# Kernel optimization log

Measured on AMD Instinct MI355X. Metric: run time of the kernel, lower is better.

The kernel has to match this reference:

```python
import jax, jax.numpy as jnp
import numpy as np

N_NODES = 50000
N_EDGES = 800000
DIM = 128


def setup_inputs() -> dict:
    key = jax.random.key(0)
    k_x, k_e, k_w1, k_w2 = jax.random.split(key, 4)
    x = jax.random.normal(k_x, (N_NODES, DIM), dtype=jnp.float32)
    edge_index = jax.random.randint(k_e, (2, N_EDGES), 0, N_NODES, dtype=jnp.int64)
    scale = 1.0 / np.sqrt(DIM)
    W1 = jax.random.normal(k_w1, (DIM, DIM), dtype=jnp.float32) * scale
    b1 = jnp.zeros((DIM,), dtype=jnp.float32)
    W2 = jax.random.normal(k_w2, (DIM, DIM), dtype=jnp.float32) * scale
    b2 = jnp.zeros((DIM,), dtype=jnp.float32)
    return {"x": x, "edge_index": edge_index, "W1": W1, "b1": b1, "W2": W2, "b2": b2}


def _gcn_conv(x, W, b, src, dst, n_nodes):
    """PyG GCNConv: D^{-1/2}(A+I)D^{-1/2} (x @ W) + b, self-loops added."""
    h = x @ W  # [N, D]
    ones = jnp.ones(src.shape[0], dtype=h.dtype)
    # degree of A+I, counting incoming edges at target nodes plus self-loop
    deg = jax.ops.segment_sum(ones, dst, num_segments=n_nodes) + 1.0
    dinv = jax.lax.rsqrt(deg)  # [N]
    norm = dinv[src] * dinv[dst]  # [E]
    msgs = h[src] * norm[:, None]  # [E, D] gather (memory-bound)
    agg = jax.ops.segment_sum(msgs, dst, num_segments=n_nodes)  # scatter-add
    agg = agg + h * (dinv * dinv)[:, None]  # self-loop contribution
    return agg + b


def reference(x, edge_index, W1, b1, W2, b2):
    src, dst = edge_index[0], edge_index[1]
    n = x.shape[0]
    identity = x
    out = jax.nn.relu(_gcn_conv(x, W1, b1, src, dst, n))
    out = _gcn_conv(out, W2, b2, src, dst, n)
    return jax.nn.relu(out + identity)
```

## Files before the change

kernel.cpp:

```cpp
#include <hip/hip_runtime.h>

#define N_NODES 50000
#define N_EDGES 800000
#define DIM 128
#define NB 391
#define CAP 2560
#define NCH 7
#define BIN_CHUNK 4096
#define BIN_BLOCKS 196
#define GEMM_TILES 782
#define AGG_TILES 1563

typedef unsigned int uint;
typedef unsigned short ushort;
typedef __attribute__((ext_vector_type(8))) __bf16 bf16x8;
typedef __attribute__((ext_vector_type(4))) float f32x4;

__device__ __forceinline__ uint f2bf(float f) {
    uint u = __float_as_uint(f);
    return (u + 0x7FFFu + ((u >> 16) & 1u)) >> 16;
}
__device__ __forceinline__ float2 bf2f2(uint u) {
    return make_float2(__uint_as_float(u << 16), __uint_as_float(u & 0xFFFF0000u));
}


__global__ __launch_bounds__(256) void prep_kernel(const float* __restrict__ W1,
                                                   const float* __restrict__ W2,
                                                   uint* __restrict__ Wt1,
                                                   uint* __restrict__ Wt2,
                                                   int* __restrict__ bincursor) {
    int idx = blockIdx.x * 256 + threadIdx.x;
    if (idx < 16384) {
        const float* W = (idx < 8192) ? W1 : W2;
        uint* Wt = (idx < 8192) ? Wt1 : Wt2;
        int i = idx & 8191;
        int n = i >> 6, k2 = i & 63;
        Wt[i] = f2bf(W[(2 * k2) * DIM + n]) | (f2bf(W[(2 * k2 + 1) * DIM + n]) << 16);
    } else {
        int b = idx - 16384;
        if (b < NB) bincursor[b] = b * CAP;
    }
}


__device__ __forceinline__ void gemm_tile64(const float* __restrict__ X,
                                            const uint* __restrict__ Wt, int base,
                                            uint* __restrict__ Hout) {
    int t = threadIdx.x;
    int wv = t >> 6;
    int l = t & 63;
    int col = l & 15;
    int g = l >> 4;
    int grow = base + wv * 16 + col;
    int ar = grow > N_NODES - 1 ? N_NODES - 1 : grow;

    bf16x8 af[4];
    const float4* Xr = (const float4*)(X + (size_t)ar * DIM);
#pragma unroll
    for (int kk = 0; kk < 4; ++kk) {
        float4 x0 = Xr[kk * 8 + g * 2];
        float4 x1 = Xr[kk * 8 + g * 2 + 1];
        uint4 p;
        p.x = f2bf(x0.x) | (f2bf(x0.y) << 16);
        p.y = f2bf(x0.z) | (f2bf(x0.w) << 16);
        p.z = f2bf(x1.x) | (f2bf(x1.y) << 16);
        p.w = f2bf(x1.z) | (f2bf(x1.w) << 16);
        af[kk] = __builtin_bit_cast(bf16x8, p);
    }

    const uint4* Wr = (const uint4*)Wt;
    f32x4 acc[8];
#pragma unroll
    for (int n = 0; n < 8; ++n) acc[n] = (f32x4){0.f, 0.f, 0.f, 0.f};

#pragma unroll
    for (int n = 0; n < 8; ++n) {
        const uint4* wrow = Wr + (size_t)(n * 16 + col) * 16;
#pragma unroll
        for (int kk = 0; kk < 4; ++kk) {
            bf16x8 bf = __builtin_bit_cast(bf16x8, wrow[kk * 4 + g]);
            acc[n] = __builtin_amdgcn_mfma_f32_16x16x32_bf16(af[kk], bf, acc[n], 0, 0, 0);
        }
    }

#pragma unroll
    for (int j = 0; j < 4; ++j) {
        int row = base + wv * 16 + g * 4 + j;
        if (row < N_NODES) {
            ushort* hrow = (ushort*)(Hout + (size_t)row * 64);
#pragma unroll
            for (int n = 0; n < 8; ++n) hrow[n * 16 + col] = (ushort)f2bf(acc[n][j]);
        }
    }
}


__device__ __forceinline__ void gemm_tile32_lds(const uint* __restrict__ sB,
                                                const uint* __restrict__ Wt,
                                                const float* __restrict__ dinv, int base,
                                                uint* __restrict__ Hout) {
    int t = threadIdx.x;
    int wv = t >> 6;
    int l = t & 63;
    int col = l & 15;
    int g = l >> 4;
    int rh = wv & 1;
    int ch = wv >> 1;
    int lr = rh * 16 + col;

    bf16x8 af[4];
#pragma unroll
    for (int kk = 0; kk < 4; ++kk) {
        int ui = lr * 64 + ((kk * 16 + g * 4) ^ ((lr & 7) << 2));
        af[kk] = __builtin_bit_cast(bf16x8, *(const uint4*)&sB[ui]);
    }

    const uint4* Wr = (const uint4*)Wt;
    f32x4 acc[4];
#pragma unroll
    for (int nn = 0; nn < 4; ++nn) acc[nn] = (f32x4){0.f, 0.f, 0.f, 0.f};

#pragma unroll
    for (int nn = 0; nn < 4; ++nn) {
        int n = ch * 4 + nn;
        const uint4* wrow = Wr + (size_t)(n * 16 + col) * 16;
#pragma unroll
        for (int kk = 0; kk < 4; ++kk) {
            bf16x8 bf = __builtin_bit_cast(bf16x8, wrow[kk * 4 + g]);
            acc[nn] = __builtin_amdgcn_mfma_f32_16x16x32_bf16(af[kk], bf, acc[nn], 0, 0, 0);
        }
    }

#pragma unroll
    for (int j = 0; j < 4; ++j) {
        int row = base + rh * 16 + g * 4 + j;
        if (row < N_NODES) {
            float di = dinv[row];
            ushort* hrow = (ushort*)(Hout + (size_t)row * 64);
#pragma unroll
            for (int nn = 0; nn < 4; ++nn) {
                int n = ch * 4 + nn;
                hrow[n * 16 + col] = (ushort)f2bf(acc[nn][j] * di);
            }
        }
    }
}


__global__ __launch_bounds__(256) void bin_gemm1_kernel(const int* __restrict__ ei,
                                                        int* __restrict__ bincursor,
                                                        uint* __restrict__ pairs,
                                                        const float* __restrict__ x,
                                                        const uint* __restrict__ Wt1,
                                                        uint* __restrict__ Hs) {
    if (blockIdx.x >= BIN_BLOCKS) {
        gemm_tile64(x, Wt1, (blockIdx.x - BIN_BLOCKS) * 64, Hs);
        return;
    }
    __shared__ int lh[NB];
    __shared__ int lbase[NB];
    int t = threadIdx.x;
    int eb = blockIdx.x * BIN_CHUNK;

    for (int b = t; b < NB; b += 256) lh[b] = 0;
    __syncthreads();

    int s_reg[16], d_reg[16];
#pragma unroll
    for (int i = 0; i < 16; ++i) {
        int e = eb + i * 256 + t;
        if (e < N_EDGES) {
            s_reg[i] = ei[e];
            d_reg[i] = ei[N_EDGES + e];
            atomicAdd(&lh[d_reg[i] >> 7], 1);
        } else {
            d_reg[i] = -1;
        }
    }
    __syncthreads();

    for (int b = t; b < NB; b += 256) {
        int c = lh[b];
        lbase[b] = c ? atomicAdd(&bincursor[b], c) : 0;
    }
    __syncthreads();
    for (int b = t; b < NB; b += 256) lh[b] = 0;
    __syncthreads();

#pragma unroll
    for (int i = 0; i < 16; ++i) {
        int d = d_reg[i];
        if (d >= 0) {
            int bin = d >> 7;
            int r = atomicAdd(&lh[bin], 1);
            pairs[lbase[bin] + r] = ((uint)s_reg[i] << 7) | (uint)(d & 127);
        }
    }
}


__global__ __launch_bounds__(256) void fill2_kernel(const uint* __restrict__ pairs,
                                                    const int* __restrict__ bincursor,
                                                    int* __restrict__ rowbeg,
                                                    int* __restrict__ rowend,
                                                    float* __restrict__ dinv,
                                                    int* __restrict__ csr_src) {
    __shared__ int cnt[128 * 8];
    __shared__ int nsum[128];
    __shared__ int nbase[128];
    int t = threadIdx.x;
    int blk = blockIdx.x;
    int bs = blk * CAP;
    int be = bincursor[blk];

    for (int i = t; i < 128 * 8; i += 256) cnt[i] = 0;
    __syncthreads();

    for (int p = bs + t; p < be; p += 256) {
        uint pr = pairs[p];
        atomicAdd(&cnt[(pr & 127u) * 8 + (pr >> 20)], 1);
    }
    __syncthreads();

    if (t < 128) {
        int s = 0;
#pragma unroll
        for (int c = 0; c < NCH; ++c) s += cnt[t * 8 + c];
        nsum[t] = s;
        nbase[t] = s;
    }
    __syncthreads();
#pragma unroll
    for (int off = 1; off < 128; off <<= 1) {
        int v = (t < 128 && t >= off) ? nbase[t - off] : 0;
        __syncthreads();
        if (t < 128) nbase[t] += v;
        __syncthreads();
    }

    if (t < 128) {
        int ex = nbase[t] - nsum[t];
        int node = blk * 128 + t;
        if (node < N_NODES) {
            rowbeg[node] = bs + ex;
            rowend[node] = bs + nbase[t];
            dinv[node] = rsqrtf((float)nsum[t] + 1.0f);
        }
        int run = ex;
#pragma unroll
        for (int c = 0; c < NCH; ++c) {
            int v = cnt[t * 8 + c];
            cnt[t * 8 + c] = run;
            run += v;
        }
    }
    __syncthreads();

    for (int p = bs + t; p < be; p += 256) {
        uint pr = pairs[p];
        int r = atomicAdd(&cnt[(pr & 127u) * 8 + (pr >> 20)], 1);
        csr_src[bs + r] = (int)(pr >> 7);
    }
}


template <bool DSRC>
__device__ __forceinline__ void agg_node(const int* __restrict__ rowbeg,
                                         const int* __restrict__ rowend,
                                         const int* __restrict__ csr_src,
                                         const uint* __restrict__ Hs,
                                         const float* __restrict__ dinv,
                                         const float* __restrict__ bias, int node, int li,
                                         float r[8]) {
    int beg = rowbeg[node];
    int end = rowend[node];
    float di = dinv[node];

    const uint4* H4 = (const uint4*)Hs;
    float a0, a1, a2, a3, a4, a5, a6, a7;
    {
        uint4 su = H4[(size_t)node * 16 + li];
        float2 v0 = bf2f2(su.x), v1 = bf2f2(su.y), v2 = bf2f2(su.z), v3 = bf2f2(su.w);
        float sf = DSRC ? di : 1.0f;
        a0 = sf * v0.x; a1 = sf * v0.y; a2 = sf * v1.x; a3 = sf * v1.y;
        a4 = sf * v2.x; a5 = sf * v2.y; a6 = sf * v3.x; a7 = sf * v3.y;
    }

#define ADDF8(u, f)                                                               \
    {                                                                             \
        float2 v0 = bf2f2(u.x), v1 = bf2f2(u.y), v2 = bf2f2(u.z), v3 = bf2f2(u.w);\
        a0 += f * v0.x; a1 += f * v0.y; a2 += f * v1.x; a3 += f * v1.y;           \
        a4 += f * v2.x; a5 += f * v2.y; a6 += f * v3.x; a7 += f * v3.y;           \
    }

    int e = beg;
    for (; e + 7 < end; e += 8) {
        int s[8];
#pragma unroll
        for (int i = 0; i < 8; ++i) s[i] = csr_src[e + i];
        uint4 u[8];
#pragma unroll
        for (int i = 0; i < 8; ++i) u[i] = H4[(size_t)s[i] * 16 + li];
        float f[8];
#pragma unroll
        for (int i = 0; i < 8; ++i) f[i] = DSRC ? dinv[s[i]] : 1.0f;
#pragma unroll
        for (int i = 0; i < 8; ++i) ADDF8(u[i], f[i]);
    }
    if (e + 3 < end) {
        int s[4];
#pragma unroll
        for (int i = 0; i < 4; ++i) s[i] = csr_src[e + i];
        uint4 u[4];
#pragma unroll
        for (int i = 0; i < 4; ++i) u[i] = H4[(size_t)s[i] * 16 + li];
        float f[4];
#pragma unroll
        for (int i = 0; i < 4; ++i) f[i] = DSRC ? dinv[s[i]] : 1.0f;
#pragma unroll
        for (int i = 0; i < 4; ++i) ADDF8(u[i], f[i]);
        e += 4;
    }
    for (; e < end; ++e) {
        int s = csr_src[e];
        uint4 u = H4[(size_t)s * 16 + li];
        float f = DSRC ? dinv[s] : 1.0f;
        ADDF8(u, f);
    }
#undef ADDF8

    const float4* B4 = (const float4*)bias;
    float4 bb0 = B4[li * 2], bb1 = B4[li * 2 + 1];
    r[0] = a0 * di + bb0.x; r[1] = a1 * di + bb0.y;
    r[2] = a2 * di + bb0.z; r[3] = a3 * di + bb0.w;
    r[4] = a4 * di + bb1.x; r[5] = a5 * di + bb1.y;
    r[6] = a6 * di + bb1.z; r[7] = a7 * di + bb1.w;
}


__global__ __launch_bounds__(256) void aggemm_kernel(const int* __restrict__ rowbeg,
                                                     const int* __restrict__ rowend,
                                                     const int* __restrict__ csr_src,
                                                     const uint* __restrict__ Hs,
                                                     const float* __restrict__ dinv,
                                                     const float* __restrict__ b1,
                                                     const uint* __restrict__ Wt2,
                                                     uint* __restrict__ Hs2) {
    __shared__ uint sB[32 * 64];
    int t = threadIdx.x;
    int wv = t >> 6;
    int lane = t & 63;
    int grp = lane >> 4;
    int li = lane & 15;
    int base = blockIdx.x * 32;

#pragma unroll
    for (int p = 0; p < 2; ++p) {
        int row = p * 16 + wv * 4 + grp;
        int node = base + row;
        if (node < N_NODES) {
            float r[8];
            agg_node<true>(rowbeg, rowend, csr_src, Hs, dinv, b1, node, li, r);
            uint4 o;
            o.x = f2bf(fmaxf(r[0], 0.f)) | (f2bf(fmaxf(r[1], 0.f)) << 16);
            o.y = f2bf(fmaxf(r[2], 0.f)) | (f2bf(fmaxf(r[3], 0.f)) << 16);
            o.z = f2bf(fmaxf(r[4], 0.f)) | (f2bf(fmaxf(r[5], 0.f)) << 16);
            o.w = f2bf(fmaxf(r[6], 0.f)) | (f2bf(fmaxf(r[7], 0.f)) << 16);
            int ui = row * 64 + ((li * 4) ^ ((row & 7) << 2));
            *(uint4*)&sB[ui] = o;
        }
    }
    __syncthreads();

    gemm_tile32_lds(sB, Wt2, dinv, base, Hs2);
}


__global__ __launch_bounds__(256) void agg2_kernel(const int* __restrict__ rowbeg,
                                                   const int* __restrict__ rowend,
                                                   const int* __restrict__ csr_src,
                                                   const uint* __restrict__ Hs2,
                                                   const float* __restrict__ dinv,
                                                   const float* __restrict__ b2,
                                                   const float* __restrict__ resid,
                                                   float* __restrict__ out) {
    int wave = (int)((blockIdx.x * (size_t)blockDim.x + threadIdx.x) >> 6);
    int lane = threadIdx.x & 63;
    int grp = lane >> 4;
    int li = lane & 15;
    int node = wave * 4 + grp;

    float r[8];
    agg_node<false>(rowbeg, rowend, csr_src, Hs2, dinv, b2, node, li, r);

    const float4* R4 = (const float4*)(resid + (size_t)node * DIM);
    float4 x0 = R4[li * 2], x1 = R4[li * 2 + 1];
    r[0] += x0.x; r[1] += x0.y; r[2] += x0.z; r[3] += x0.w;
    r[4] += x1.x; r[5] += x1.y; r[6] += x1.z; r[7] += x1.w;

    float4* O4 = (float4*)(out + (size_t)node * DIM);
    O4[li * 2] = make_float4(fmaxf(r[0], 0.f), fmaxf(r[1], 0.f), fmaxf(r[2], 0.f),
                             fmaxf(r[3], 0.f));
    O4[li * 2 + 1] = make_float4(fmaxf(r[4], 0.f), fmaxf(r[5], 0.f), fmaxf(r[6], 0.f),
                                 fmaxf(r[7], 0.f));
}


extern "C" void kernel_launch(void* const* d_in, const int* in_sizes, int n_in,
                              void* d_out, int out_size, void* d_ws, size_t ws_size,
                              hipStream_t stream) {
    const float* x = (const float*)d_in[0];
    const int* edge_index = (const int*)d_in[1];
    const float* W1 = (const float*)d_in[2];
    const float* b1 = (const float*)d_in[3];
    const float* W2 = (const float*)d_in[4];
    const float* b2 = (const float*)d_in[5];
    float* out = (float*)d_out;

    char* ws = (char*)d_ws;
    int*   bincursor = (int*)(ws + 0);
    float* dinv      = (float*)(ws + (64 << 10));
    int*   rowbeg    = (int*)(ws + (320 << 10));
    int*   rowend    = (int*)(ws + (576 << 10));
    int*   csr_src   = (int*)(ws + (1 << 20));
    uint*  pairs     = (uint*)(ws + (6 << 20));
    uint*  Hs        = (uint*)(ws + (11 << 20));
    uint*  Hs2       = (uint*)(ws + (24 << 20));
    uint*  Wt1       = (uint*)(ws + (37 << 20));
    uint*  Wt2       = (uint*)(ws + (37 << 20) + (64 << 10));

    prep_kernel<<<66, 256, 0, stream>>>(W1, W2, Wt1, Wt2, bincursor);
    bin_gemm1_kernel<<<BIN_BLOCKS + GEMM_TILES, 256, 0, stream>>>(edge_index, bincursor, pairs,
                                                                  x, Wt1, Hs);
    fill2_kernel<<<NB, 256, 0, stream>>>(pairs, bincursor, rowbeg, rowend, dinv, csr_src);
    aggemm_kernel<<<AGG_TILES, 256, 0, stream>>>(rowbeg, rowend, csr_src, Hs, dinv, b1, Wt2,
                                                 Hs2);
    agg2_kernel<<<3125, 256, 0, stream>>>(rowbeg, rowend, csr_src, Hs2, dinv, b2, x, out);
}
```

Before: 123.6 us.

## Split hidden features into column panels for cache-friendly gather aggregation

Stores the bf16 hidden matrices as four 32-column panels and runs aggregation as one block per (tile, panel), so each gather pass touches a smaller working set that fits better in L2/MALL. The fused aggregate+GEMM2 kernel is split back into a separate panel aggregation and a standalone GEMM2 kernel reading the panelled layout. In exchange, edge indices and row bounds are re-read once per panel, each gathered row segment shrinks to 64 bytes, and an extra kernel launch plus an intermediate round-trip are added.

```diff
diff --git a/kernel.cpp b/kernel.cpp
--- a/kernel.cpp
+++ b/kernel.cpp
@@ -9,7 +9,8 @@
 #define BIN_CHUNK 4096
 #define BIN_BLOCKS 196
 #define GEMM_TILES 782
-#define AGG_TILES 1563
+#define AGG_TILES 782
+#define NPANEL 4
 
 typedef unsigned int uint;
 typedef unsigned short ushort;
@@ -44,9 +45,10 @@
 }
 
 
+
 __device__ __forceinline__ void gemm_tile64(const float* __restrict__ X,
                                             const uint* __restrict__ Wt, int base,
-                                            uint* __restrict__ Hout) {
+                                            uint* __restrict__ HP) {
     int t = threadIdx.x;
     int wv = t >> 6;
     int l = t & 63;
@@ -84,64 +86,15 @@
         }
     }
 
+    ushort* Hp = (ushort*)HP;
 #pragma unroll
     for (int j = 0; j < 4; ++j) {
         int row = base + wv * 16 + g * 4 + j;
         if (row < N_NODES) {
-            ushort* hrow = (ushort*)(Hout + (size_t)row * 64);
-#pragma unroll
-            for (int n = 0; n < 8; ++n) hrow[n * 16 + col] = (ushort)f2bf(acc[n][j]);
-        }
-    }
-}
-
-
-__device__ __forceinline__ void gemm_tile32_lds(const uint* __restrict__ sB,
-                                                const uint* __restrict__ Wt,
-                                                const float* __restrict__ dinv, int base,
-                                                uint* __restrict__ Hout) {
-    int t = threadIdx.x;
-    int wv = t >> 6;
-    int l = t & 63;
-    int col = l & 15;
-    int g = l >> 4;
-    int rh = wv & 1;
-    int ch = wv >> 1;
-    int lr = rh * 16 + col;
-
-    bf16x8 af[4];
-#pragma unroll
-    for (int kk = 0; kk < 4; ++kk) {
-        int ui = lr * 64 + ((kk * 16 + g * 4) ^ ((lr & 7) << 2));
-        af[kk] = __builtin_bit_cast(bf16x8, *(const uint4*)&sB[ui]);
-    }
-
-    const uint4* Wr = (const uint4*)Wt;
-    f32x4 acc[4];
-#pragma unroll
-    for (int nn = 0; nn < 4; ++nn) acc[nn] = (f32x4){0.f, 0.f, 0.f, 0.f};
-
-#pragma unroll
-    for (int nn = 0; nn < 4; ++nn) {
-        int n = ch * 4 + nn;
-        const uint4* wrow = Wr + (size_t)(n * 16 + col) * 16;
-#pragma unroll
-        for (int kk = 0; kk < 4; ++kk) {
-            bf16x8 bf = __builtin_bit_cast(bf16x8, wrow[kk * 4 + g]);
-            acc[nn] = __builtin_amdgcn_mfma_f32_16x16x32_bf16(af[kk], bf, acc[nn], 0, 0, 0);
-        }
-    }
-
-#pragma unroll
-    for (int j = 0; j < 4; ++j) {
-        int row = base + rh * 16 + g * 4 + j;
-        if (row < N_NODES) {
-            float di = dinv[row];
-            ushort* hrow = (ushort*)(Hout + (size_t)row * 64);
-#pragma unroll
-            for (int nn = 0; nn < 4; ++nn) {
-                int n = ch * 4 + nn;
-                hrow[n * 16 + col] = (ushort)f2bf(acc[nn][j] * di);
+#pragma unroll
+            for (int n = 0; n < 8; ++n) {
+                Hp[((size_t)((n >> 1) * N_NODES + row)) * 32 + (n & 1) * 16 + col] =
+                    (ushort)f2bf(acc[n][j]);
             }
         }
     }
@@ -153,9 +106,9 @@
                                                         uint* __restrict__ pairs,
                                                         const float* __restrict__ x,
                                                         const uint* __restrict__ Wt1,
-                                                        uint* __restrict__ Hs) {
+                                                        uint* __restrict__ HP) {
     if (blockIdx.x >= BIN_BLOCKS) {
-        gemm_tile64(x, Wt1, (blockIdx.x - BIN_BLOCKS) * 64, Hs);
+        gemm_tile64(x, Wt1, (blockIdx.x - BIN_BLOCKS) * 64, HP);
         return;
     }
     __shared__ int lh[NB];
@@ -265,22 +218,36 @@
 }
 
 
-template <bool DSRC>
-__device__ __forceinline__ void agg_node(const int* __restrict__ rowbeg,
-                                         const int* __restrict__ rowend,
-                                         const int* __restrict__ csr_src,
-                                         const uint* __restrict__ Hs,
-                                         const float* __restrict__ dinv,
-                                         const float* __restrict__ bias, int node, int li,
-                                         float r[8]) {
-    int beg = rowbeg[node];
-    int end = rowend[node];
-    float di = dinv[node];
-
-    const uint4* H4 = (const uint4*)Hs;
+template <bool DSRC, bool OBF>
+__global__ __launch_bounds__(256) void aggP_kernel(const int* __restrict__ rowbeg,
+                                                   const int* __restrict__ rowend,
+                                                   const int* __restrict__ csr_src,
+                                                   const uint* __restrict__ HP,
+                                                   const float* __restrict__ dinv,
+                                                   const float* __restrict__ bias,
+                                                   const float* __restrict__ resid,
+                                                   void* __restrict__ outv) {
+    int bid = blockIdx.x;
+    int panel = bid & 3;
+    int tile = bid >> 2;
+    int t = threadIdx.x;
+    int wv = t >> 6;
+    int l = t & 63;
+    int sub = l >> 2;
+    int li = l & 3;
+    int node = tile * 64 + wv * 16 + sub;
+    bool valid = node < N_NODES;
+    int nn = valid ? node : N_NODES - 1;
+
+    int beg = rowbeg[nn];
+    int end = valid ? rowend[nn] : beg;
+    float di = dinv[nn];
+
+    const uint4* H = (const uint4*)HP + (size_t)panel * (N_NODES * 4);
+
     float a0, a1, a2, a3, a4, a5, a6, a7;
     {
-        uint4 su = H4[(size_t)node * 16 + li];
+        uint4 su = H[(size_t)nn * 4 + li];
         float2 v0 = bf2f2(su.x), v1 = bf2f2(su.y), v2 = bf2f2(su.z), v3 = bf2f2(su.w);
         float sf = DSRC ? di : 1.0f;
         a0 = sf * v0.x; a1 = sf * v0.y; a2 = sf * v1.x; a3 = sf * v1.y;
@@ -301,7 +268,7 @@
         for (int i = 0; i < 8; ++i) s[i] = csr_src[e + i];
         uint4 u[8];
 #pragma unroll
-        for (int i = 0; i < 8; ++i) u[i] = H4[(size_t)s[i] * 16 + li];
+        for (int i = 0; i < 8; ++i) u[i] = H[(size_t)s[i] * 4 + li];
         float f[8];
 #pragma unroll
         for (int i = 0; i < 8; ++i) f[i] = DSRC ? dinv[s[i]] : 1.0f;
@@ -314,7 +281,7 @@
         for (int i = 0; i < 4; ++i) s[i] = csr_src[e + i];
         uint4 u[4];
 #pragma unroll
-        for (int i = 0; i < 4; ++i) u[i] = H4[(size_t)s[i] * 16 + li];
+        for (int i = 0; i < 4; ++i) u[i] = H[(size_t)s[i] * 4 + li];
         float f[4];
 #pragma unroll
         for (int i = 0; i < 4; ++i) f[i] = DSRC ? dinv[s[i]] : 1.0f;
@@ -324,86 +291,88 @@
     }
     for (; e < end; ++e) {
         int s = csr_src[e];
-        uint4 u = H4[(size_t)s * 16 + li];
+        uint4 u = H[(size_t)s * 4 + li];
         float f = DSRC ? dinv[s] : 1.0f;
         ADDF8(u, f);
     }
 #undef ADDF8
 
-    const float4* B4 = (const float4*)bias;
-    float4 bb0 = B4[li * 2], bb1 = B4[li * 2 + 1];
-    r[0] = a0 * di + bb0.x; r[1] = a1 * di + bb0.y;
-    r[2] = a2 * di + bb0.z; r[3] = a3 * di + bb0.w;
-    r[4] = a4 * di + bb1.x; r[5] = a5 * di + bb1.y;
-    r[6] = a6 * di + bb1.z; r[7] = a7 * di + bb1.w;
-}
-
-
-__global__ __launch_bounds__(256) void aggemm_kernel(const int* __restrict__ rowbeg,
-                                                     const int* __restrict__ rowend,
-                                                     const int* __restrict__ csr_src,
-                                                     const uint* __restrict__ Hs,
-                                                     const float* __restrict__ dinv,
-                                                     const float* __restrict__ b1,
-                                                     const uint* __restrict__ Wt2,
-                                                     uint* __restrict__ Hs2) {
-    __shared__ uint sB[32 * 64];
+    if (!valid) return;
+
+    const float4* B4 = (const float4*)(bias + panel * 32 + li * 8);
+    float4 bb0 = B4[0], bb1 = B4[1];
+    float r0 = a0 * di + bb0.x, r1 = a1 * di + bb0.y;
+    float r2 = a2 * di + bb0.z, r3 = a3 * di + bb0.w;
+    float r4 = a4 * di + bb1.x, r5 = a5 * di + bb1.y;
+    float r6 = a6 * di + bb1.z, r7 = a7 * di + bb1.w;
+
+    if (OBF) {
+        uint4 o;
+        o.x = f2bf(fmaxf(r0, 0.f)) | (f2bf(fmaxf(r1, 0.f)) << 16);
+        o.y = f2bf(fmaxf(r2, 0.f)) | (f2bf(fmaxf(r3, 0.f)) << 16);
+        o.z = f2bf(fmaxf(r4, 0.f)) | (f2bf(fmaxf(r5, 0.f)) << 16);
+        o.w = f2bf(fmaxf(r6, 0.f)) | (f2bf(fmaxf(r7, 0.f)) << 16);
+        ((uint4*)outv)[(size_t)(panel * N_NODES + node) * 4 + li] = o;
+    } else {
+        const float4* R4 = (const float4*)(resid + (size_t)node * DIM + panel * 32 + li * 8);
+        float4 x0 = R4[0], x1 = R4[1];
+        r0 += x0.x; r1 += x0.y; r2 += x0.z; r3 += x0.w;
+        r4 += x1.x; r5 += x1.y; r6 += x1.z; r7 += x1.w;
+        float4* O4 = (float4*)((float*)outv + (size_t)node * DIM + panel * 32 + li * 8);
+        O4[0] = make_float4(fmaxf(r0, 0.f), fmaxf(r1, 0.f), fmaxf(r2, 0.f), fmaxf(r3, 0.f));
+        O4[1] = make_float4(fmaxf(r4, 0.f), fmaxf(r5, 0.f), fmaxf(r6, 0.f), fmaxf(r7, 0.f));
+    }
+}
+
+
+__global__ __launch_bounds__(256) void gemm2_kernel(const uint* __restrict__ out1P,
+                                                    const uint* __restrict__ Wt,
+                                                    const float* __restrict__ dinv,
+                                                    uint* __restrict__ HP) {
     int t = threadIdx.x;
     int wv = t >> 6;
-    int lane = t & 63;
-    int grp = lane >> 4;
-    int li = lane & 15;
-    int base = blockIdx.x * 32;
-
-#pragma unroll
-    for (int p = 0; p < 2; ++p) {
-        int row = p * 16 + wv * 4 + grp;
-        int node = base + row;
-        if (node < N_NODES) {
-            float r[8];
-            agg_node<true>(rowbeg, rowend, csr_src, Hs, dinv, b1, node, li, r);
-            uint4 o;
-            o.x = f2bf(fmaxf(r[0], 0.f)) | (f2bf(fmaxf(r[1], 0.f)) << 16);
-            o.y = f2bf(fmaxf(r[2], 0.f)) | (f2bf(fmaxf(r[3], 0.f)) << 16);
-            o.z = f2bf(fmaxf(r[4], 0.f)) | (f2bf(fmaxf(r[5], 0.f)) << 16);
-            o.w = f2bf(fmaxf(r[6], 0.f)) | (f2bf(fmaxf(r[7], 0.f)) << 16);
-            int ui = row * 64 + ((li * 4) ^ ((row & 7) << 2));
-            *(uint4*)&sB[ui] = o;
-        }
-    }
-    __syncthreads();
-
-    gemm_tile32_lds(sB, Wt2, dinv, base, Hs2);
-}
-
-
-__global__ __launch_bounds__(256) void agg2_kernel(const int* __restrict__ rowbeg,
-                                                   const int* __restrict__ rowend,
-                                                   const int* __restrict__ csr_src,
-                                                   const uint* __restrict__ Hs2,
-                                                   const float* __restrict__ dinv,
-                                                   const float* __restrict__ b2,
-                                                   const float* __restrict__ resid,
-                                                   float* __restrict__ out) {
-    int wave = (int)((blockIdx.x * (size_t)blockDim.x + threadIdx.x) >> 6);
-    int lane = threadIdx.x & 63;
-    int grp = lane >> 4;
-    int li = lane & 15;
-    int node = wave * 4 + grp;
-
-    float r[8];
-    agg_node<false>(rowbeg, rowend, csr_src, Hs2, dinv, b2, node, li, r);
-
-    const float4* R4 = (const float4*)(resid + (size_t)node * DIM);
-    float4 x0 = R4[li * 2], x1 = R4[li * 2 + 1];
-    r[0] += x0.x; r[1] += x0.y; r[2] += x0.z; r[3] += x0.w;
-    r[4] += x1.x; r[5] += x1.y; r[6] += x1.z; r[7] += x1.w;
-
-    float4* O4 = (float4*)(out + (size_t)node * DIM);
-    O4[li * 2] = make_float4(fmaxf(r[0], 0.f), fmaxf(r[1], 0.f), fmaxf(r[2], 0.f),
-                             fmaxf(r[3], 0.f));
-    O4[li * 2 + 1] = make_float4(fmaxf(r[4], 0.f), fmaxf(r[5], 0.f), fmaxf(r[6], 0.f),
-                                 fmaxf(r[7], 0.f));
+    int l = t & 63;
+    int col = l & 15;
+    int g = l >> 4;
+    int base = blockIdx.x * 64;
+    int grow = base + wv * 16 + col;
+    int ar = grow > N_NODES - 1 ? N_NODES - 1 : grow;
+
+    bf16x8 af[4];
+#pragma unroll
+    for (int kk = 0; kk < 4; ++kk) {
+        af[kk] = __builtin_bit_cast(
+            bf16x8, *(const uint4*)(out1P + ((size_t)(kk * N_NODES + ar)) * 16 + g * 4));
+    }
+
+    const uint4* Wr = (const uint4*)Wt;
+    f32x4 acc[8];
+#pragma unroll
+    for (int n = 0; n < 8; ++n) acc[n] = (f32x4){0.f, 0.f, 0.f, 0.f};
+
+#pragma unroll
+    for (int n = 0; n < 8; ++n) {
+        const uint4* wrow = Wr + (size_t)(n * 16 + col) * 16;
+#pragma unroll
+        for (int kk = 0; kk < 4; ++kk) {
+            bf16x8 bf = __builtin_bit_cast(bf16x8, wrow[kk * 4 + g]);
+            acc[n] = __builtin_amdgcn_mfma_f32_16x16x32_bf16(af[kk], bf, acc[n], 0, 0, 0);
+        }
+    }
+
+    ushort* Hp = (ushort*)HP;
+#pragma unroll
+    for (int j = 0; j < 4; ++j) {
+        int row = base + wv * 16 + g * 4 + j;
+        if (row < N_NODES) {
+            float di = dinv[row];
+#pragma unroll
+            for (int n = 0; n < 8; ++n) {
+                Hp[((size_t)((n >> 1) * N_NODES + row)) * 32 + (n & 1) * 16 + col] =
+                    (ushort)f2bf(acc[n][j] * di);
+            }
+        }
+    }
 }
 
 
@@ -425,16 +394,18 @@
     int*   rowend    = (int*)(ws + (576 << 10));
     int*   csr_src   = (int*)(ws + (1 << 20));
     uint*  pairs     = (uint*)(ws + (6 << 20));
-    uint*  Hs        = (uint*)(ws + (11 << 20));
-    uint*  Hs2       = (uint*)(ws + (24 << 20));
+    uint*  HsP       = (uint*)(ws + (11 << 20));
+    uint*  out1P     = (uint*)(ws + (24 << 20));
     uint*  Wt1       = (uint*)(ws + (37 << 20));
     uint*  Wt2       = (uint*)(ws + (37 << 20) + (64 << 10));
 
     prep_kernel<<<66, 256, 0, stream>>>(W1, W2, Wt1, Wt2, bincursor);
     bin_gemm1_kernel<<<BIN_BLOCKS + GEMM_TILES, 256, 0, stream>>>(edge_index, bincursor, pairs,
-                                                                  x, Wt1, Hs);
+                                                                  x, Wt1, HsP);
     fill2_kernel<<<NB, 256, 0, stream>>>(pairs, bincursor, rowbeg, rowend, dinv, csr_src);
-    aggemm_kernel<<<AGG_TILES, 256, 0, stream>>>(rowbeg, rowend, csr_src, Hs, dinv, b1, Wt2,
-                                                 Hs2);
-    agg2_kernel<<<3125, 256, 0, stream>>>(rowbeg, rowend, csr_src, Hs2, dinv, b2, x, out);
-}
+    aggP_kernel<true, true><<<AGG_TILES * NPANEL, 256, 0, stream>>>(
+        rowbeg, rowend, csr_src, HsP, dinv, b1, nullptr, (void*)out1P);
+    gemm2_kernel<<<GEMM_TILES, 256, 0, stream>>>(out1P, Wt2, dinv, HsP);
+    aggP_kernel<false, false><<<AGG_TILES * NPANEL, 256, 0, stream>>>(
+        rowbeg, rowend, csr_src, HsP, dinv, b2, x, (void*)out);
+}
```

New measurement: 140.4 us. 1.14x slower.
